# Kernel tuning notes

Hardware: AMD Instinct MI355X
Metric: run time of the kernel (lower is better)

The kernel has to match this reference:

```python
import jax, jax.numpy as jnp
import numpy as np
from jax import lax

GN_GROUPS = 8
GN_EPS = 1e-5
K_BITS = 8
DELTA = 0.05
EPS = 1e-8


def setup_inputs() -> dict:
    key = jax.random.key(0)
    k1, k2 = jax.random.split(key)
    B, Cin, H, W = 32, 256, 56, 56
    Cout, KS = 256, 3
    x = jax.random.normal(k1, (B, Cin, H, W), dtype=jnp.float32)
    # kaiming_normal_(nonlinearity='relu'): std = sqrt(2 / fan_in)
    fan_in = Cin * KS * KS
    weight_fp = jax.random.normal(k2, (Cout, Cin, KS, KS), dtype=jnp.float32) * np.sqrt(2.0 / fan_in)
    gamma = jnp.ones((Cin,), dtype=jnp.float32)
    beta = jnp.zeros((Cin,), dtype=jnp.float32)
    a = jnp.asarray(6.0, dtype=jnp.float32)  # PACT learnable clip
    bias = jnp.zeros((Cout,), dtype=jnp.float32)
    return {"x": x, "gamma": gamma, "beta": beta, "a": a, "weight_fp": weight_fp, "bias": bias}


def _group_norm(x, gamma, beta):
    B, C, H, W = x.shape
    xg = x.reshape(B, GN_GROUPS, -1)
    mu = xg.mean(axis=-1, keepdims=True)
    var = xg.var(axis=-1, keepdims=True)  # biased, matches torch GroupNorm
    xn = ((xg - mu) * lax.rsqrt(var + GN_EPS)).reshape(B, C, H, W)
    return xn * gamma[:, None, None] + beta[:, None, None]


def _pact_quant(x, a):
    a_c = jnp.maximum(a, 0.0) + EPS
    S = (2.0 ** K_BITS - 1.0) / a_c
    y = jnp.clip(x, 0.0, a_c)
    # straight-through round
    return y + lax.stop_gradient(jnp.round(y * S) / S - y)


def _ternary_weight(w_r):
    oc = w_r.shape[0]
    wv = w_r.reshape(oc, -1)
    wa = jnp.abs(wv)
    t = DELTA * wa.mean(axis=1, keepdims=True)
    m = (wa > t).astype(wv.dtype)
    alpha = (wa * m).sum(axis=1, keepdims=True) / (m.sum(axis=1, keepdims=True) + EPS)
    wq = (alpha * jnp.sign(wv) * m).reshape(w_r.shape)
    # STE gradient factor: m + 0.5*(1 - m)
    g = lax.stop_gradient((0.5 + 0.5 * m).reshape(w_r.shape))
    return g * w_r + lax.stop_gradient(wq - g * w_r)


def reference(x, gamma, beta, a, weight_fp, bias):
    h = _group_norm(x, gamma, beta)
    h = jnp.maximum(h, 0.0) ** 2          # ReLU^2
    h = _pact_quant(h, a)                  # PACT k-bit uniform quant
    w = _ternary_weight(weight_fp)         # ternary {-alpha, 0, +alpha}
    out = lax.conv_general_dilated(
        h, w, window_strides=(1, 1), padding=[(1, 1), (1, 1)],
        dimension_numbers=("NCHW", "OIHW", "NCHW"))
    return out + bias[:, None, None]
```

## Files before the change

kernel.cpp:

```cpp
#include <hip/hip_runtime.h>
#include <hip/hip_bf16.h>

#define B_    32
#define C_    256
#define H_    56
#define W_    56
#define HW_   3136
#define P_    58
#define G_    8
#define COUT_ 256
#define KTOT_ 2304

typedef _Float16 h16;
typedef _Float16 half8 __attribute__((ext_vector_type(8)));
typedef _Float16 h16x4 __attribute__((ext_vector_type(4)));
typedef float    f32x4 __attribute__((ext_vector_type(4)));

__global__ __launch_bounds__(1024)
void gn_stats_kernel(const float* __restrict__ x, float* __restrict__ stats) {
    int bg = blockIdx.x;
    const float4* base = (const float4*)(x + (size_t)bg * (32 * HW_));
    float s1 = 0.f, s2 = 0.f;
    for (int i = threadIdx.x; i < 25088; i += 1024) {
        float4 v = base[i];
        s1 += v.x + v.y + v.z + v.w;
        s2 += v.x * v.x + v.y * v.y + v.z * v.z + v.w * v.w;
    }
    #pragma unroll
    for (int off = 32; off; off >>= 1) {
        s1 += __shfl_down(s1, off, 64);
        s2 += __shfl_down(s2, off, 64);
    }
    __shared__ float ra[16], rb[16];
    int lane = threadIdx.x & 63, wv = threadIdx.x >> 6;
    if (!lane) { ra[wv] = s1; rb[wv] = s2; }
    __syncthreads();
    if (threadIdx.x == 0) {
        float t1 = 0.f, t2 = 0.f;
        #pragma unroll
        for (int i = 0; i < 16; ++i) { t1 += ra[i]; t2 += rb[i]; }
        float mu = t1 / 100352.f;
        float var = t2 / 100352.f - mu * mu;
        stats[bg * 2]     = mu;
        stats[bg * 2 + 1] = rsqrtf(var + 1e-5f);
    }
}

__global__ __launch_bounds__(256)
void act_kernel(const float* __restrict__ x, const float* __restrict__ gamma,
                const float* __restrict__ beta, const float* __restrict__ a_ptr,
                const float* __restrict__ stats, h16* __restrict__ q) {
    int by = blockIdx.x;
    int b = by / P_;
    int y = by - b * P_;
    h16* qrow = q + (size_t)by * P_ * C_;
    if (y == 0 || y == P_ - 1) {
        for (int i = threadIdx.x; i < P_ * C_; i += 256) qrow[i] = (h16)0.f;
        return;
    }
    __shared__ h16 T[256][64];

    int t = threadIdx.x;
    float a_c = fmaxf(a_ptr[0], 0.f) + 1e-8f;
    float S   = 255.f / a_c;

    int j  = t & 15;
    int cb = t >> 4;
    #pragma unroll 4
    for (int iter = 0; iter < 16; ++iter) {
        int ci = iter * 16 + cb;
        if (j < 14) {
            int g = ci >> 5;
            float mu = stats[(b * G_ + g) * 2];
            float rs = stats[(b * G_ + g) * 2 + 1];
            float ga = gamma[ci], be = beta[ci];
            const float4* xr = (const float4*)(x + ((size_t)(b * C_ + ci)) * HW_ + (y - 1) * W_);
            float4 v = xr[j];
            h16x4 o;
            float f[4] = {v.x, v.y, v.z, v.w};
            #pragma unroll
            for (int s = 0; s < 4; ++s) {
                float yv = (f[s] - mu) * rs * ga + be;
                float r  = fmaxf(yv, 0.f);
                float h2 = fminf(r * r, a_c);
                o[s] = (h16)rintf(h2 * S);
            }
            *(h16x4*)&T[ci][((j + ci) & 15) * 4] = o;
        }
    }
    __syncthreads();

    int c = t;
    qrow[c] = (h16)0.f;
    qrow[(P_ - 1) * C_ + c] = (h16)0.f;
    #pragma unroll
    for (int jb = 0; jb < 14; ++jb) {
        h16x4 v = *(const h16x4*)&T[c][((jb + c) & 15) * 4];
        #pragma unroll
        for (int s = 0; s < 4; ++s)
            qrow[(jb * 4 + s + 1) * C_ + c] = v[s];
    }
}

__global__ __launch_bounds__(256)
void wq_kernel(const float* __restrict__ wfp, h16* __restrict__ wt,
               float* __restrict__ alphas) {
    int oc = blockIdx.x;
    int t  = threadIdx.x;
    const float* wr = wfp + (size_t)oc * KTOT_;
    float wl[9];
    float s = 0.f;
    #pragma unroll
    for (int j = 0; j < 9; ++j) { wl[j] = wr[t + j * 256]; s += fabsf(wl[j]); }

    __shared__ float red[4];
    int lane = t & 63, wv = t >> 6;
    #pragma unroll
    for (int off = 32; off; off >>= 1) s += __shfl_down(s, off, 64);
    if (!lane) red[wv] = s;
    __syncthreads();
    float thr = 0.05f * ((red[0] + red[1] + red[2] + red[3]) / (float)KTOT_);
    __syncthreads();

    float sm = 0.f, cnt = 0.f;
    #pragma unroll
    for (int j = 0; j < 9; ++j) {
        float aw = fabsf(wl[j]);
        if (aw > thr) { sm += aw; cnt += 1.f; }
    }
    #pragma unroll
    for (int off = 32; off; off >>= 1) {
        sm  += __shfl_down(sm, off, 64);
        cnt += __shfl_down(cnt, off, 64);
    }
    __shared__ float redc[4];
    if (!lane) { red[wv] = sm; redc[wv] = cnt; }
    __syncthreads();
    if (t == 0) {
        float alpha = (red[0] + red[1] + red[2] + red[3]) /
                      (redc[0] + redc[1] + redc[2] + redc[3] + 1e-8f);
        alphas[oc] = alpha;
    }
    #pragma unroll
    for (int j = 0; j < 9; ++j) {
        int i  = t + j * 256;
        int ic = i / 9;
        int tap = i - ic * 9;
        float w = wl[j];
        float tern = (fabsf(w) > thr) ? (w > 0.f ? 1.f : -1.f) : 0.f;
        wt[((size_t)tap * 256 + oc) * 256 + ic] = (h16)tern;
    }
}

__global__ __launch_bounds__(512)
void conv_gemm_kernel(const h16* __restrict__ q, const h16* __restrict__ wt,
                      const float* __restrict__ alphas, const float* __restrict__ bias,
                      const float* __restrict__ a_ptr, float* __restrict__ out) {
    int mt = blockIdx.x;
    int tid = threadIdx.x;
    int lane = tid & 63;
    int wv = tid >> 6;
    int wm = wv & 1, wn = wv >> 1;
    int quad = lane >> 4, lrow = lane & 15;

    __shared__ h16 As[128 * 64];
    __shared__ h16 Bs[256 * 64];

    int kswz = (((tid & 7) ^ ((tid >> 3) & 7)) << 3);
    int sb[2], wb[4];
    #pragma unroll
    for (int r = 0; r < 2; ++r) {
        int ml = r * 64 + (tid >> 3);
        int m = mt * 128 + ml;
        int b = m / HW_;
        int rem = m - b * HW_;
        int hh = rem / W_;
        int ww = rem - hh * W_;
        sb[r] = ((b * P_ + hh + 1) * P_ + (ww + 1)) * C_ + kswz;
    }
    #pragma unroll
    for (int r = 0; r < 4; ++r) {
        int oc = r * 64 + (tid >> 3);
        wb[r] = oc * C_ + kswz;
    }

    f32x4 acc[4][4];
    #pragma unroll
    for (int i = 0; i < 4; ++i)
        #pragma unroll
        for (int j = 0; j < 4; ++j) { acc[i][j][0]=0.f; acc[i][j][1]=0.f; acc[i][j][2]=0.f; acc[i][j][3]=0.f; }

    int arow = wm * 64 + lrow;
    int brow = wn * 64 + lrow;
    int rsw = lrow & 7;

    for (int kk = 0; kk < 36; ++kk) {
        int tap = kk >> 2;
        int ic0 = (kk & 3) << 6;
        int dh = tap / 3 - 1;
        int dw = tap - (tap / 3) * 3 - 1;
        int aoff = (dh * P_ + dw) * C_ + ic0;
        const h16* gb = wt + (size_t)tap * (256 * 256) + ic0;
        #pragma unroll
        for (int r = 0; r < 2; ++r) {
            __builtin_amdgcn_global_load_lds(
                (const __attribute__((address_space(1))) void*)(q + sb[r] + aoff),
                (__attribute__((address_space(3))) void*)(&As[r * 4096 + tid * 8]),
                16, 0, 0);
        }
        #pragma unroll
        for (int r = 0; r < 4; ++r) {
            __builtin_amdgcn_global_load_lds(
                (const __attribute__((address_space(1))) void*)(gb + wb[r]),
                (__attribute__((address_space(3))) void*)(&Bs[r * 4096 + tid * 8]),
                16, 0, 0);
        }
        __syncthreads();
        #pragma unroll
        for (int ks = 0; ks < 2; ++ks) {
            int cb = (ks * 4 + quad) ^ rsw;
            half8 af[4], bf[4];
            #pragma unroll
            for (int mi = 0; mi < 4; ++mi)
                af[mi] = *(const half8*)&As[(arow + mi * 16) * 64 + cb * 8];
            #pragma unroll
            for (int ni = 0; ni < 4; ++ni)
                bf[ni] = *(const half8*)&Bs[(brow + ni * 16) * 64 + cb * 8];
            #pragma unroll
            for (int mi = 0; mi < 4; ++mi)
                #pragma unroll
                for (int ni = 0; ni < 4; ++ni)
                    acc[mi][ni] = __builtin_amdgcn_mfma_f32_16x16x32_f16(
                        af[mi], bf[ni], acc[mi][ni], 0, 0, 0);
        }
        __syncthreads();
    }

    float a_c = fmaxf(a_ptr[0], 0.f) + 1e-8f;
    float qs  = a_c * (1.f / 255.f);
    #pragma unroll
    for (int ni = 0; ni < 4; ++ni) {
        int n = wn * 64 + ni * 16 + lrow;
        float sc = alphas[n] * qs;
        float bn = bias[n];
        #pragma unroll
        for (int mi = 0; mi < 4; ++mi) {
            int mbase = mt * 128 + wm * 64 + mi * 16 + quad * 4;
            int b = mbase / HW_;
            size_t off = (size_t)b * (C_ * HW_) + (size_t)n * HW_ + (mbase - b * HW_);
            f32x4 v;
            #pragma unroll
            for (int r = 0; r < 4; ++r) v[r] = acc[mi][ni][r] * sc + bn;
            *(f32x4*)(out + off) = v;
        }
    }
}

extern "C" void kernel_launch(void* const* d_in, const int* in_sizes, int n_in,
                              void* d_out, int out_size, void* d_ws, size_t ws_size,
                              hipStream_t stream) {
    const float* x     = (const float*)d_in[0];
    const float* gamma = (const float*)d_in[1];
    const float* beta  = (const float*)d_in[2];
    const float* a     = (const float*)d_in[3];
    const float* wfp   = (const float*)d_in[4];
    const float* bias  = (const float*)d_in[5];
    float* out = (float*)d_out;

    char* ws = (char*)d_ws;
    h16*  qbuf   = (h16*)ws;
    h16*  wtb    = (h16*)(ws + 55115776);
    float* alphas = (float*)(ws + 55115776 + 1179648);
    float* stats  = alphas + 256;

    gn_stats_kernel<<<B_ * G_, 1024, 0, stream>>>(x, stats);
    wq_kernel<<<COUT_, 256, 0, stream>>>(wfp, wtb, alphas);
    act_kernel<<<B_ * P_, 256, 0, stream>>>(x, gamma, beta, a, stats, qbuf);
    conv_gemm_kernel<<<784, 512, 0, stream>>>(qbuf, wtb, alphas, bias, a, out);
}
```

Baseline: 325.7 us.

## Switch conv GEMM to int8 MFMA with offset-shifted activations and correction

Activations (0..255 codes) are stored as int8 shifted by -128 and ternary weights as int8. The conv GEMM then uses i32 16x16x64 int8 MFMA with half the K iterations. A per-output-channel sum of ternary signs adds back the 128 offset in the epilogue, and padding is set to -128 so that it maps to zero. The act kernel is rewritten to pack 4 channels per int and drops the LDS transpose. This halves activation and weight bytes and doubles MFMA throughput per instruction, and stays exact because integer accumulation cannot overflow.

Measured after the change: 290.8 us. 1.12x faster.

```diff
diff --git a/kernel.cpp b/kernel.cpp
--- a/kernel.cpp
+++ b/kernel.cpp
@@ -11,10 +11,8 @@
 #define COUT_ 256
 #define KTOT_ 2304
 
-typedef _Float16 h16;
-typedef _Float16 half8 __attribute__((ext_vector_type(8)));
-typedef _Float16 h16x4 __attribute__((ext_vector_type(4)));
-typedef float    f32x4 __attribute__((ext_vector_type(4)));
+typedef float f32x4 __attribute__((ext_vector_type(4)));
+typedef int   i32x4 __attribute__((ext_vector_type(4)));
 
 __global__ __launch_bounds__(1024)
 void gn_stats_kernel(const float* __restrict__ x, float* __restrict__ stats) {
@@ -49,62 +47,64 @@
 __global__ __launch_bounds__(256)
 void act_kernel(const float* __restrict__ x, const float* __restrict__ gamma,
                 const float* __restrict__ beta, const float* __restrict__ a_ptr,
-                const float* __restrict__ stats, h16* __restrict__ q) {
+                const float* __restrict__ stats, char* __restrict__ q) {
     int by = blockIdx.x;
     int b = by / P_;
     int y = by - b * P_;
-    h16* qrow = q + (size_t)by * P_ * C_;
+    char* qrow = q + (size_t)by * P_ * C_;
+    const int PADV = 0x80808080;
     if (y == 0 || y == P_ - 1) {
-        for (int i = threadIdx.x; i < P_ * C_; i += 256) qrow[i] = (h16)0.f;
+        int4 pv = {PADV, PADV, PADV, PADV};
+        for (int i = threadIdx.x; i < (P_ * C_) / 16; i += 256)
+            ((int4*)qrow)[i] = pv;
         return;
     }
-    __shared__ h16 T[256][64];
-
     int t = threadIdx.x;
+    if (t < 64)            ((int*)qrow)[t] = PADV;
+    else if (t < 128)      ((int*)(qrow + (P_ - 1) * C_))[t - 64] = PADV;
+
     float a_c = fmaxf(a_ptr[0], 0.f) + 1e-8f;
     float S   = 255.f / a_c;
 
-    int j  = t & 15;
-    int cb = t >> 4;
-    #pragma unroll 4
-    for (int iter = 0; iter < 16; ++iter) {
-        int ci = iter * 16 + cb;
-        if (j < 14) {
-            int g = ci >> 5;
-            float mu = stats[(b * G_ + g) * 2];
-            float rs = stats[(b * G_ + g) * 2 + 1];
-            float ga = gamma[ci], be = beta[ci];
-            const float4* xr = (const float4*)(x + ((size_t)(b * C_ + ci)) * HW_ + (y - 1) * W_);
-            float4 v = xr[j];
-            h16x4 o;
-            float f[4] = {v.x, v.y, v.z, v.w};
+    int c4 = t & 63;
+    int wb = t >> 6;
+    int g  = (4 * c4) >> 5;
+    float mu = stats[(b * G_ + g) * 2];
+    float rs = stats[(b * G_ + g) * 2 + 1];
+    float ga[4], be[4];
+    #pragma unroll
+    for (int i = 0; i < 4; ++i) { ga[i] = gamma[4 * c4 + i]; be[i] = beta[4 * c4 + i]; }
+
+    const float* xb = x + ((size_t)(b * C_ + 4 * c4)) * HW_ + (y - 1) * W_;
+    for (int j = wb; j < 14; j += 4) {
+        float4 v[4];
+        #pragma unroll
+        for (int i = 0; i < 4; ++i)
+            v[i] = *(const float4*)(xb + (size_t)i * HW_ + j * 4);
+        int qv[4][4];
+        #pragma unroll
+        for (int i = 0; i < 4; ++i) {
+            float f[4] = {v[i].x, v[i].y, v[i].z, v[i].w};
             #pragma unroll
             for (int s = 0; s < 4; ++s) {
-                float yv = (f[s] - mu) * rs * ga + be;
+                float yv = (f[s] - mu) * rs * ga[i] + be[i];
                 float r  = fmaxf(yv, 0.f);
                 float h2 = fminf(r * r, a_c);
-                o[s] = (h16)rintf(h2 * S);
+                qv[i][s] = (int)rintf(h2 * S) - 128;
             }
-            *(h16x4*)&T[ci][((j + ci) & 15) * 4] = o;
-        }
-    }
-    __syncthreads();
-
-    int c = t;
-    qrow[c] = (h16)0.f;
-    qrow[(P_ - 1) * C_ + c] = (h16)0.f;
-    #pragma unroll
-    for (int jb = 0; jb < 14; ++jb) {
-        h16x4 v = *(const h16x4*)&T[c][((jb + c) & 15) * 4];
-        #pragma unroll
-        for (int s = 0; s < 4; ++s)
-            qrow[(jb * 4 + s + 1) * C_ + c] = v[s];
+        }
+        #pragma unroll
+        for (int s = 0; s < 4; ++s) {
+            int packed = (qv[0][s] & 255) | ((qv[1][s] & 255) << 8) |
+                         ((qv[2][s] & 255) << 16) | (qv[3][s] << 24);
+            *(int*)(qrow + (j * 4 + s + 1) * C_ + 4 * c4) = packed;
+        }
     }
 }
 
 __global__ __launch_bounds__(256)
-void wq_kernel(const float* __restrict__ wfp, h16* __restrict__ wt,
-               float* __restrict__ alphas) {
+void wq_kernel(const float* __restrict__ wfp, char* __restrict__ wt,
+               float* __restrict__ alphas, float* __restrict__ tsum) {
     int oc = blockIdx.x;
     int t  = threadIdx.x;
     const float* wr = wfp + (size_t)oc * KTOT_;
@@ -122,24 +122,29 @@
     float thr = 0.05f * ((red[0] + red[1] + red[2] + red[3]) / (float)KTOT_);
     __syncthreads();
 
-    float sm = 0.f, cnt = 0.f;
+    float sm = 0.f, cnt = 0.f, ts = 0.f;
     #pragma unroll
     for (int j = 0; j < 9; ++j) {
         float aw = fabsf(wl[j]);
-        if (aw > thr) { sm += aw; cnt += 1.f; }
+        if (aw > thr) {
+            sm += aw; cnt += 1.f;
+            ts += (wl[j] > 0.f) ? 1.f : -1.f;
+        }
     }
     #pragma unroll
     for (int off = 32; off; off >>= 1) {
         sm  += __shfl_down(sm, off, 64);
         cnt += __shfl_down(cnt, off, 64);
-    }
-    __shared__ float redc[4];
-    if (!lane) { red[wv] = sm; redc[wv] = cnt; }
+        ts  += __shfl_down(ts, off, 64);
+    }
+    __shared__ float redc[4], redt[4];
+    if (!lane) { red[wv] = sm; redc[wv] = cnt; redt[wv] = ts; }
     __syncthreads();
     if (t == 0) {
         float alpha = (red[0] + red[1] + red[2] + red[3]) /
                       (redc[0] + redc[1] + redc[2] + redc[3] + 1e-8f);
         alphas[oc] = alpha;
+        tsum[oc] = redt[0] + redt[1] + redt[2] + redt[3];
     }
     #pragma unroll
     for (int j = 0; j < 9; ++j) {
@@ -147,15 +152,16 @@
         int ic = i / 9;
         int tap = i - ic * 9;
         float w = wl[j];
-        float tern = (fabsf(w) > thr) ? (w > 0.f ? 1.f : -1.f) : 0.f;
-        wt[((size_t)tap * 256 + oc) * 256 + ic] = (h16)tern;
+        char tern = (fabsf(w) > thr) ? (w > 0.f ? (char)1 : (char)-1) : (char)0;
+        wt[((size_t)tap * 256 + oc) * 256 + ic] = tern;
     }
 }
 
 __global__ __launch_bounds__(512)
-void conv_gemm_kernel(const h16* __restrict__ q, const h16* __restrict__ wt,
+void conv_gemm_kernel(const char* __restrict__ q, const char* __restrict__ wt,
                       const float* __restrict__ alphas, const float* __restrict__ bias,
-                      const float* __restrict__ a_ptr, float* __restrict__ out) {
+                      const float* __restrict__ tsum, const float* __restrict__ a_ptr,
+                      float* __restrict__ out) {
     int mt = blockIdx.x;
     int tid = threadIdx.x;
     int lane = tid & 63;
@@ -163,10 +169,10 @@
     int wm = wv & 1, wn = wv >> 1;
     int quad = lane >> 4, lrow = lane & 15;
 
-    __shared__ h16 As[128 * 64];
-    __shared__ h16 Bs[256 * 64];
-
-    int kswz = (((tid & 7) ^ ((tid >> 3) & 7)) << 3);
+    __shared__ char As[128 * 128];
+    __shared__ char Bs[256 * 128];
+
+    int kswz = (((tid & 7) ^ ((tid >> 3) & 7)) << 4);
     int sb[2], wb[4];
     #pragma unroll
     for (int r = 0; r < 2; ++r) {
@@ -184,53 +190,53 @@
         wb[r] = oc * C_ + kswz;
     }
 
-    f32x4 acc[4][4];
+    i32x4 acc[4][4];
     #pragma unroll
     for (int i = 0; i < 4; ++i)
         #pragma unroll
-        for (int j = 0; j < 4; ++j) { acc[i][j][0]=0.f; acc[i][j][1]=0.f; acc[i][j][2]=0.f; acc[i][j][3]=0.f; }
+        for (int j = 0; j < 4; ++j) { acc[i][j][0]=0; acc[i][j][1]=0; acc[i][j][2]=0; acc[i][j][3]=0; }
 
     int arow = wm * 64 + lrow;
     int brow = wn * 64 + lrow;
     int rsw = lrow & 7;
 
-    for (int kk = 0; kk < 36; ++kk) {
-        int tap = kk >> 2;
-        int ic0 = (kk & 3) << 6;
+    for (int kk = 0; kk < 18; ++kk) {
+        int tap = kk >> 1;
+        int ic0 = (kk & 1) << 7;
         int dh = tap / 3 - 1;
         int dw = tap - (tap / 3) * 3 - 1;
         int aoff = (dh * P_ + dw) * C_ + ic0;
-        const h16* gb = wt + (size_t)tap * (256 * 256) + ic0;
+        const char* gb = wt + (size_t)tap * (256 * 256) + ic0;
         #pragma unroll
         for (int r = 0; r < 2; ++r) {
             __builtin_amdgcn_global_load_lds(
                 (const __attribute__((address_space(1))) void*)(q + sb[r] + aoff),
-                (__attribute__((address_space(3))) void*)(&As[r * 4096 + tid * 8]),
+                (__attribute__((address_space(3))) void*)(&As[r * 8192 + tid * 16]),
                 16, 0, 0);
         }
         #pragma unroll
         for (int r = 0; r < 4; ++r) {
             __builtin_amdgcn_global_load_lds(
                 (const __attribute__((address_space(1))) void*)(gb + wb[r]),
-                (__attribute__((address_space(3))) void*)(&Bs[r * 4096 + tid * 8]),
+                (__attribute__((address_space(3))) void*)(&Bs[r * 8192 + tid * 16]),
                 16, 0, 0);
         }
         __syncthreads();
         #pragma unroll
         for (int ks = 0; ks < 2; ++ks) {
             int cb = (ks * 4 + quad) ^ rsw;
-            half8 af[4], bf[4];
+            i32x4 af[4], bf[4];
             #pragma unroll
             for (int mi = 0; mi < 4; ++mi)
-                af[mi] = *(const half8*)&As[(arow + mi * 16) * 64 + cb * 8];
+                af[mi] = *(const i32x4*)&As[(arow + mi * 16) * 128 + cb * 16];
             #pragma unroll
             for (int ni = 0; ni < 4; ++ni)
-                bf[ni] = *(const half8*)&Bs[(brow + ni * 16) * 64 + cb * 8];
+                bf[ni] = *(const i32x4*)&Bs[(brow + ni * 16) * 128 + cb * 16];
             #pragma unroll
             for (int mi = 0; mi < 4; ++mi)
                 #pragma unroll
                 for (int ni = 0; ni < 4; ++ni)
-                    acc[mi][ni] = __builtin_amdgcn_mfma_f32_16x16x32_f16(
+                    acc[mi][ni] = __builtin_amdgcn_mfma_i32_16x16x64_i8(
                         af[mi], bf[ni], acc[mi][ni], 0, 0, 0);
         }
         __syncthreads();
@@ -243,6 +249,7 @@
         int n = wn * 64 + ni * 16 + lrow;
         float sc = alphas[n] * qs;
         float bn = bias[n];
+        float corr = 128.f * tsum[n];
         #pragma unroll
         for (int mi = 0; mi < 4; ++mi) {
             int mbase = mt * 128 + wm * 64 + mi * 16 + quad * 4;
@@ -250,7 +257,8 @@
             size_t off = (size_t)b * (C_ * HW_) + (size_t)n * HW_ + (mbase - b * HW_);
             f32x4 v;
             #pragma unroll
-            for (int r = 0; r < 4; ++r) v[r] = acc[mi][ni][r] * sc + bn;
+            for (int r = 0; r < 4; ++r)
+                v[r] = ((float)acc[mi][ni][r] + corr) * sc + bn;
             *(f32x4*)(out + off) = v;
         }
     }
@@ -268,13 +276,14 @@
     float* out = (float*)d_out;
 
     char* ws = (char*)d_ws;
-    h16*  qbuf   = (h16*)ws;
-    h16*  wtb    = (h16*)(ws + 55115776);
-    float* alphas = (float*)(ws + 55115776 + 1179648);
-    float* stats  = alphas + 256;
+    char*  qbuf   = ws;
+    char*  wtb    = ws + 27557888;
+    float* alphas = (float*)(ws + 27557888 + 589824);
+    float* tsum   = alphas + 256;
+    float* stats  = tsum + 256;
 
     gn_stats_kernel<<<B_ * G_, 1024, 0, stream>>>(x, stats);
-    wq_kernel<<<COUT_, 256, 0, stream>>>(wfp, wtb, alphas);
+    wq_kernel<<<COUT_, 256, 0, stream>>>(wfp, wtb, alphas, tsum);
     act_kernel<<<B_ * P_, 256, 0, stream>>>(x, gamma, beta, a, stats, qbuf);
-    conv_gemm_kernel<<<784, 512, 0, stream>>>(qbuf, wtb, alphas, bias, a, out);
-}
+    conv_gemm_kernel<<<784, 512, 0, stream>>>(qbuf, wtb, alphas, bias, tsum, a, out);
+}
```
